# Performance work log

Measured on AMD Instinct MI355X. Metric: run time of the kernel, lower is better.

## Reference

```python
import jax, jax.numpy as jnp
import numpy as np

B, T, D_IN, H, NC = 256, 512, 40, 128, 7


def _lstm_dir(x, W_ih, W_hh, b):
    # x: [B,T,D]; W_ih: [4H,D]; W_hh: [4H,H]; b: [4H] (b_ih+b_hh combined)
    pre = jnp.einsum('btd,gd->btg', x, W_ih) + b  # [B,T,4H]
    h0 = jnp.zeros((x.shape[0], W_hh.shape[1]), x.dtype)
    c0 = jnp.zeros_like(h0)

    def step(carry, p_t):
        h, c = carry
        g = p_t + h @ W_hh.T  # [B,4H]
        i, f, gg, o = jnp.split(g, 4, axis=-1)  # PyTorch gate order: i,f,g,o
        i = jax.nn.sigmoid(i)
        f = jax.nn.sigmoid(f)
        gg = jnp.tanh(gg)
        o = jax.nn.sigmoid(o)
        c = f * c + i * gg
        h = o * jnp.tanh(c)
        return (h, c), h

    _, hs = jax.lax.scan(step, (h0, c0), jnp.swapaxes(pre, 0, 1))  # [T,B,H]
    return jnp.swapaxes(hs, 0, 1)  # [B,T,H]


def _bilstm_layer(x, Wf, Uf, bf, Wr, Ur, br):
    fwd = _lstm_dir(x, Wf, Uf, bf)
    rev = _lstm_dir(x[:, ::-1], Wr, Ur, br)[:, ::-1]
    return jnp.concatenate([fwd, rev], axis=-1)  # [B,T,2H]


def setup_inputs() -> dict:
    key = jax.random.key(0)
    ks = jax.random.split(key, 20)
    s = 1.0 / np.sqrt(H)  # PyTorch LSTM init scale

    def u(k, shape):
        return jax.random.uniform(k, shape, jnp.float32, -s, s)

    inp = {
        'x': jax.random.normal(ks[0], (B, T, D_IN), jnp.float32),
        # layer 0 (input dim 40)
        'W_ih_l0_f': u(ks[1], (4 * H, D_IN)), 'W_hh_l0_f': u(ks[2], (4 * H, H)), 'b_l0_f': u(ks[3], (4 * H,)),
        'W_ih_l0_r': u(ks[4], (4 * H, D_IN)), 'W_hh_l0_r': u(ks[5], (4 * H, H)), 'b_l0_r': u(ks[6], (4 * H,)),
        # layer 1 (input dim 2H)
        'W_ih_l1_f': u(ks[7], (4 * H, 2 * H)), 'W_hh_l1_f': u(ks[8], (4 * H, H)), 'b_l1_f': u(ks[9], (4 * H,)),
        'W_ih_l1_r': u(ks[10], (4 * H, 2 * H)), 'W_hh_l1_r': u(ks[11], (4 * H, H)), 'b_l1_r': u(ks[12], (4 * H,)),
        # classifier head
        'fc_w': u(ks[13], (NC, 2 * H)), 'fc_b': u(ks[14], (NC,)),
    }
    return inp


def reference(x, W_ih_l0_f, W_hh_l0_f, b_l0_f, W_ih_l0_r, W_hh_l0_r, b_l0_r,
              W_ih_l1_f, W_hh_l1_f, b_l1_f, W_ih_l1_r, W_hh_l1_r, b_l1_r,
              fc_w, fc_b):
    h1 = _bilstm_layer(x, W_ih_l0_f, W_hh_l0_f, b_l0_f, W_ih_l0_r, W_hh_l0_r, b_l0_r)
    h2 = _bilstm_layer(h1, W_ih_l1_f, W_hh_l1_f, b_l1_f, W_ih_l1_r, W_hh_l1_r, b_l1_r)
    last = h2[:, -1, :]  # [B,2H]; dropout is identity at eval time
    return last @ fc_w.T + fc_b  # [B,NC]
```

## Files before the change

kernel.cpp:

```cpp
#include <hip/hip_runtime.h>
#include <hip/hip_bf16.h>
#include <type_traits>

typedef short short8 __attribute__((ext_vector_type(8)));
typedef short short4v __attribute__((ext_vector_type(4)));
typedef float f32x4 __attribute__((ext_vector_type(4)));
typedef __bf16 bf16x8 __attribute__((ext_vector_type(8)));

#define DEVI static __device__ __forceinline__

#if __has_builtin(__builtin_amdgcn_exp2f)
#define EXP2(x) __builtin_amdgcn_exp2f(x)
#else
#define EXP2(x) exp2f(x)
#endif
#if __has_builtin(__builtin_amdgcn_rcpf)
#define RCP(x) __builtin_amdgcn_rcpf(x)
#else
#define RCP(x) (1.0f / (x))
#endif

static constexpr int BB = 256, TT = 512, DIN0 = 40, HH = 128, NCLS = 7;
static constexpr float L2E = 1.44269504088896f;

DEVI short f2b(float x) {
  union { __hip_bfloat16 h; short s; } u;
  u.h = __float2bfloat16(x);
  return u.s;
}
DEVI bf16x8 as_bf(short8 s) { return __builtin_bit_cast(bf16x8, s); }
DEVI float b2f(short s) {
  union { unsigned u; float f; } v;
  v.u = ((unsigned)(unsigned short)s) << 16;
  return v.f;
}

DEVI void bar_lgkm() {
  asm volatile("s_waitcnt lgkmcnt(0)\n\ts_barrier" ::: "memory");
}

DEVI f32x4 inv4(f32x4 d) {
  float p1 = d[0] * d[1];
  float p2 = p1 * d[2];
  float p3 = p2 * d[3];
  float R = RCP(p3);
  f32x4 r;
  r[3] = R * p2;
  float R2 = R * d[3];
  r[2] = R2 * p1;
  float R1 = R2 * d[2];
  r[1] = R1 * d[0];
  r[0] = R1 * d[1];
  return r;
}

__global__ __launch_bounds__(512) void rec0(
    const float* __restrict__ x0,
    const float* __restrict__ Wih_f, const float* __restrict__ Whh_f,
    const float* __restrict__ b_f, const float* __restrict__ Wih_r,
    const float* __restrict__ Whh_r, const float* __restrict__ b_r,
    short* __restrict__ h1_out) {
  __shared__ short Hb[2][16][16][8];
  __shared__ short X2[2][8][16][8];

  const int tid = threadIdx.x, w = tid >> 6, lane = tid & 63;
  const int lg = lane >> 4, bcol = lane & 15;
  const int dir = blockIdx.x & 1, b0 = (blockIdx.x >> 1) * 16;
  const int j0 = w * 16 + lg * 4;
  const float* __restrict__ Wih = dir ? Wih_r : Wih_f;
  const float* __restrict__ Whh = dir ? Whh_r : Whh_f;
  const float* __restrict__ bias = dir ? b_r : b_f;
  auto tmap = [&](int s) { return dir ? (TT - 1 - s) : s; };

  short8 wx[4][2], wh[4][4];
  f32x4 bq[4];
#pragma unroll
  for (int q = 0; q < 4; ++q) {
    const float scale = (q == 2) ? (2.0f * L2E) : (-L2E);
    const int m = q * HH + w * 16 + bcol;
#pragma unroll
    for (int kk = 0; kk < 2; ++kk) {
      short8 f;
#pragma unroll
      for (int e = 0; e < 8; ++e) {
        const int k = kk * 32 + lg * 8 + e;
        float v = (k < DIN0) ? Wih[(size_t)m * DIN0 + k] : 0.0f;
        f[e] = f2b(v * scale);
      }
      wx[q][kk] = f;
    }
#pragma unroll
    for (int kk = 0; kk < 4; ++kk) {
      short8 f;
#pragma unroll
      for (int e = 0; e < 8; ++e)
        f[e] = f2b(Whh[(size_t)m * HH + kk * 32 + lg * 8 + e] * scale);
      wh[q][kk] = f;
    }
#pragma unroll
    for (int r = 0; r < 4; ++r) bq[q][r] = bias[q * HH + j0 + r] * scale;
  }

  for (int i = tid; i < 2 * 16 * 16 * 4; i += 512) ((int*)Hb)[i] = 0;
  for (int i = tid; i < 2 * 8 * 16 * 4; i += 512) ((int*)X2)[i] = 0;
  __syncthreads();

  auto load_x = [&](int s) -> f32x4 {
    f32x4 v = {0.f, 0.f, 0.f, 0.f};
    if (tid < 160) {
      int ss = (s < TT) ? s : (TT - 1);
      v = *(const f32x4*)(x0 + ((size_t)(b0 + tid / 10) * TT + tmap(ss)) * DIN0 + (tid % 10) * 4);
    }
    return v;
  };
  auto stage_x = [&](int buf, const f32x4& v) {
    if (tid < 160) {
      short4v o;
      o[0] = f2b(v[0]); o[1] = f2b(v[1]); o[2] = f2b(v[2]); o[3] = f2b(v[3]);
      const int row = tid / 10, c4 = tid % 10;
      *(short4v*)&X2[buf][c4 >> 1][row][(c4 & 1) * 4] = o;
    }
  };
  auto prefill = [&](f32x4* acc, int p) {
#pragma unroll
    for (int kk = 0; kk < 2; ++kk) {
      const bf16x8 bx = as_bf(*(const short8*)&X2[p][kk * 4 + lg][bcol][0]);
#pragma unroll
      for (int q = 0; q < 4; ++q)
        acc[q] = __builtin_amdgcn_mfma_f32_16x16x32_bf16(
            as_bf(wx[q][kk]), bx, (kk == 0) ? bq[q] : acc[q], 0, 0, 0);
    }
  };

  f32x4 cst = {0.f, 0.f, 0.f, 0.f};
  auto cell = [&](f32x4* a, int cur, int s) {
    f32x4 Ei, Ef, Eg, Eo;
#pragma unroll
    for (int r = 0; r < 4; ++r) {
      Ei[r] = EXP2(fminf(a[0][r], 30.f));
      Ef[r] = EXP2(fminf(a[1][r], 30.f));
      Eg[r] = EXP2(fminf(a[2][r], 30.f));
      Eo[r] = EXP2(fminf(a[3][r], 30.f));
    }
    const f32x4 one = {1.f, 1.f, 1.f, 1.f};
    f32x4 si = inv4(one + Ei), sf = inv4(one + Ef);
    f32x4 gd = inv4(one + Eg), so = inv4(one + Eo);
    f32x4 Ec;
#pragma unroll
    for (int r = 0; r < 4; ++r) {
      float tg = 1.f - 2.f * gd[r];
      cst[r] = sf[r] * cst[r] + si[r] * tg;
      Ec[r] = EXP2(fminf(cst[r] * (2.f * L2E), 30.f));
    }
    f32x4 cd = inv4(one + Ec);
    short4v hp;
#pragma unroll
    for (int r = 0; r < 4; ++r) hp[r] = f2b(so[r] * (1.f - 2.f * cd[r]));
    *(short4v*)&Hb[cur ^ 1][j0 >> 3][bcol][j0 & 7] = hp;
    *(short4v*)(h1_out + (((size_t)(b0 + bcol) * TT + tmap(s)) << 8) + dir * HH + j0) = hp;
  };

  stage_x(0, load_x(0));
  stage_x(1, load_x(1));
  f32x4 xst = load_x(2);
  __syncthreads();
  f32x4 accA[4], accB[4];
  prefill(accA, 0);
  bar_lgkm();

  auto stepf = [&](int s, int cur, f32x4* acc, f32x4* accN) {
#pragma unroll
    for (int kk = 0; kk < 4; ++kk) {
      const bf16x8 bh = as_bf(*(const short8*)&Hb[cur][kk * 4 + lg][bcol][0]);
#pragma unroll
      for (int q = 0; q < 4; ++q)
        acc[q] = __builtin_amdgcn_mfma_f32_16x16x32_bf16(as_bf(wh[q][kk]), bh, acc[q], 0, 0, 0);
    }
    cell(acc, cur, s);
    stage_x(cur, xst);
    xst = load_x(s + 3);
    prefill(accN, cur ^ 1);
    bar_lgkm();
  };
  for (int s = 0; s < TT; s += 2) {
    stepf(s, 0, accA, accB);
    stepf(s + 1, 1, accB, accA);
  }
}

template <typename PT>
__global__ __launch_bounds__(512) void pre1(
    const short* __restrict__ h1, const float* __restrict__ Wih_f,
    const float* __restrict__ b_f, const float* __restrict__ Wih_r,
    const float* __restrict__ b_r, PT* __restrict__ pre) {
  __shared__ short X[16 * 256];
  const int tid = threadIdx.x, w = tid >> 6, lane = tid & 63;
  const int lg = lane >> 4, bcol = lane & 15;
  const int gid = blockIdx.x;
  const int dir = gid & 1, tc = (gid >> 1) & 63, bt = gid >> 7;
  const float* __restrict__ Wih = dir ? Wih_r : Wih_f;
  const float* __restrict__ bias = dir ? b_r : b_f;
  const int b0 = bt * 16;

  short8 wx[4][8];
  f32x4 bq[4];
#pragma unroll
  for (int q = 0; q < 4; ++q) {
    const float scale = (q == 2) ? (2.0f * L2E) : (-L2E);
    const int m = q * HH + w * 16 + bcol;
#pragma unroll
    for (int kk = 0; kk < 8; ++kk) {
      short8 f;
#pragma unroll
      for (int e = 0; e < 8; ++e)
        f[e] = f2b(Wih[(size_t)m * 256 + kk * 32 + lg * 8 + e] * scale);
      wx[q][kk] = f;
    }
#pragma unroll
    for (int r = 0; r < 4; ++r) bq[q][r] = bias[q * HH + w * 16 + lg * 4 + r] * scale;
  }

  const int srow = tid >> 5, sch = tid & 31;
  for (int i = 0; i < 8; ++i) {
    const int t = tc * 8 + i;
    short8 v = *(const short8*)(h1 + (((size_t)(b0 + srow) * TT + t) << 8) + sch * 8);
    *(short8*)((char*)X + srow * 512 + ((sch * 16) ^ ((srow & 7) << 4))) = v;
    __syncthreads();
    f32x4 acc[4] = {bq[0], bq[1], bq[2], bq[3]};
#pragma unroll
    for (int kk = 0; kk < 8; ++kk) {
      const bf16x8 bx = as_bf(*(const short8*)((const char*)X + bcol * 512 +
                                               ((kk * 64 + lg * 16) ^ ((bcol & 7) << 4))));
#pragma unroll
      for (int q = 0; q < 4; ++q)
        acc[q] = __builtin_amdgcn_mfma_f32_16x16x32_bf16(as_bf(wx[q][kk]), bx, acc[q], 0, 0, 0);
    }
    PT* op = pre + ((((size_t)dir * 16 + bt) * TT + t) * 8 + w) * 1024 +
             (size_t)(lg * 16 + bcol) * 4;
#pragma unroll
    for (int q = 0; q < 4; ++q) {
      if constexpr (std::is_same_v<PT, float>) {
        *(f32x4*)(op + q * 256) = acc[q];
      } else {
        short4v o;
        o[0] = f2b(acc[q][0]); o[1] = f2b(acc[q][1]);
        o[2] = f2b(acc[q][2]); o[3] = f2b(acc[q][3]);
        *(short4v*)(op + q * 256) = o;
      }
    }
    __syncthreads();
  }
}

template <typename PT>
__global__ __launch_bounds__(512) void rec1(
    const PT* __restrict__ pre, const float* __restrict__ Whh_f,
    const float* __restrict__ Whh_r, float* __restrict__ h2last) {
  __shared__ short Hb[2][16][16][8];
  const int tid = threadIdx.x, w = tid >> 6, lane = tid & 63;
  const int lg = lane >> 4, bcol = lane & 15;
  const int dir = blockIdx.x & 1, bt = blockIdx.x >> 1;
  const int b0 = bt * 16, j0 = w * 16 + lg * 4;
  const float* __restrict__ Whh = dir ? Whh_r : Whh_f;
  auto tmap = [&](int s) { return dir ? (TT - 1 - s) : s; };

  short8 wh[4][4];
#pragma unroll
  for (int q = 0; q < 4; ++q) {
    const float scale = (q == 2) ? (2.0f * L2E) : (-L2E);
    const int m = q * HH + w * 16 + bcol;
#pragma unroll
    for (int kk = 0; kk < 4; ++kk) {
      short8 f;
#pragma unroll
      for (int e = 0; e < 8; ++e)
        f[e] = f2b(Whh[(size_t)m * HH + kk * 32 + lg * 8 + e] * scale);
      wh[q][kk] = f;
    }
  }
  for (int i = tid; i < 2 * 16 * 16 * 4; i += 512) ((int*)Hb)[i] = 0;
  __syncthreads();

  const size_t laneoff = (size_t)(lg * 16 + bcol) * 4;
  auto loadp = [&](f32x4* p, int s) {
    int ss = (s < TT) ? s : (TT - 1);
    const PT* base = pre + ((((size_t)dir * 16 + bt) * TT + tmap(ss)) * 8 + w) * 1024 + laneoff;
#pragma unroll
    for (int q = 0; q < 4; ++q) {
      if constexpr (std::is_same_v<PT, float>) {
        p[q] = *(const f32x4*)(base + q * 256);
      } else {
        short4v v = *(const short4v*)(base + q * 256);
        p[q][0] = b2f(v[0]); p[q][1] = b2f(v[1]);
        p[q][2] = b2f(v[2]); p[q][3] = b2f(v[3]);
      }
    }
  };

  f32x4 cst = {0.f, 0.f, 0.f, 0.f};
  auto stepf = [&](int s, int cur, f32x4* pX) {
    f32x4 acc[4] = {pX[0], pX[1], pX[2], pX[3]};
#pragma unroll
    for (int kk = 0; kk < 4; ++kk) {
      const bf16x8 bh = as_bf(*(const short8*)&Hb[cur][kk * 4 + lg][bcol][0]);
#pragma unroll
      for (int q = 0; q < 4; ++q)
        acc[q] = __builtin_amdgcn_mfma_f32_16x16x32_bf16(as_bf(wh[q][kk]), bh, acc[q], 0, 0, 0);
    }
    f32x4 Ei, Ef, Eg, Eo;
#pragma unroll
    for (int r = 0; r < 4; ++r) {
      Ei[r] = EXP2(fminf(acc[0][r], 30.f));
      Ef[r] = EXP2(fminf(acc[1][r], 30.f));
      Eg[r] = EXP2(fminf(acc[2][r], 30.f));
      Eo[r] = EXP2(fminf(acc[3][r], 30.f));
    }
    const f32x4 one = {1.f, 1.f, 1.f, 1.f};
    f32x4 si = inv4(one + Ei), sf = inv4(one + Ef);
    f32x4 gd = inv4(one + Eg), so = inv4(one + Eo);
    f32x4 Ec;
#pragma unroll
    for (int r = 0; r < 4; ++r) {
      float tg = 1.f - 2.f * gd[r];
      cst[r] = sf[r] * cst[r] + si[r] * tg;
      Ec[r] = EXP2(fminf(cst[r] * (2.f * L2E), 30.f));
    }
    f32x4 cd = inv4(one + Ec);
    short4v hp;
    f32x4 hf;
#pragma unroll
    for (int r = 0; r < 4; ++r) {
      float hv = so[r] * (1.f - 2.f * cd[r]);
      hf[r] = hv;
      hp[r] = f2b(hv);
    }
    *(short4v*)&Hb[cur ^ 1][j0 >> 3][bcol][j0 & 7] = hp;
    if ((dir == 0 && s == TT - 1) || (dir == 1 && s == 0))
      *(f32x4*)(h2last + ((size_t)(b0 + bcol) << 8) + dir * HH + j0) = hf;
    loadp(pX, s + 2);
    bar_lgkm();
  };

  f32x4 pA[4], pB[4];
  loadp(pA, 0);
  loadp(pB, 1);
  for (int s = 0; s < TT; s += 2) {
    stepf(s, 0, pA);
    stepf(s + 1, 1, pB);
  }
}

__global__ __launch_bounds__(512) void rec1_fused(
    const short* __restrict__ h1, const float* __restrict__ Wih_f,
    const float* __restrict__ Whh_f, const float* __restrict__ b_f,
    const float* __restrict__ Wih_r, const float* __restrict__ Whh_r,
    const float* __restrict__ b_r, float* __restrict__ h2last) {
  __shared__ short Hb[2][16][16][8];
  __shared__ char Xraw[16384];

  const int tid = threadIdx.x, w = tid >> 6, lane = tid & 63;
  const int lg = lane >> 4, bcol = lane & 15;
  const int dir = blockIdx.x & 1, b0 = (blockIdx.x >> 1) * 16;
  const int j0 = w * 16 + lg * 4;
  const float* __restrict__ Wih = dir ? Wih_r : Wih_f;
  const float* __restrict__ Whh = dir ? Whh_r : Whh_f;
  const float* __restrict__ bias = dir ? b_r : b_f;
  auto tmap = [&](int s) { return dir ? (TT - 1 - s) : s; };

  short8 wx[4][8], wh[4][4];
  f32x4 bq[4];
#pragma unroll
  for (int q = 0; q < 4; ++q) {
    const float scale = (q == 2) ? (2.0f * L2E) : (-L2E);
    const int m = q * HH + w * 16 + bcol;
#pragma unroll
    for (int kk = 0; kk < 8; ++kk) {
      short8 f;
#pragma unroll
      for (int e = 0; e < 8; ++e)
        f[e] = f2b(Wih[(size_t)m * 256 + kk * 32 + lg * 8 + e] * scale);
      wx[q][kk] = f;
    }
#pragma unroll
    for (int kk = 0; kk < 4; ++kk) {
      short8 f;
#pragma unroll
      for (int e = 0; e < 8; ++e)
        f[e] = f2b(Whh[(size_t)m * HH + kk * 32 + lg * 8 + e] * scale);
      wh[q][kk] = f;
    }
#pragma unroll
    for (int r = 0; r < 4; ++r) bq[q][r] = bias[q * HH + j0 + r] * scale;
  }
  for (int i = tid; i < 2 * 16 * 16 * 4; i += 512) ((int*)Hb)[i] = 0;
  __syncthreads();

  const int xr1 = tid >> 5;
  const int xcb = ((tid << 4) ^ (((tid >> 5) & 7) << 4)) & 511;
  auto ldx = [&](int p, int kk) -> short8 {
    int byte = ((bcol << 9) + (kk << 6) + (lg << 4)) ^ ((bcol & 7) << 4);
    return *(const short8*)(Xraw + p * 8192 + byte);
  };
  auto ldg = [&](int s) -> short8 {
    int ss = (s < TT) ? s : (TT - 1);
    return *(const short8*)((const char*)h1 + (((size_t)(b0 + xr1) * TT + tmap(ss)) << 9) + xcb);
  };

  {
    short8 v0 = ldg(0), v1 = ldg(1);
    *(short8*)(Xraw + tid * 16) = v0;
    *(short8*)(Xraw + 8192 + tid * 16) = v1;
  }
  short8 xstage = ldg(2);
  __syncthreads();

  f32x4 acc[4] = {bq[0], bq[1], bq[2], bq[3]};
#pragma unroll
  for (int kk = 0; kk < 8; ++kk) {
    bf16x8 bx = as_bf(ldx(0, kk));
#pragma unroll
    for (int q = 0; q < 4; ++q)
      acc[q] = __builtin_amdgcn_mfma_f32_16x16x32_bf16(as_bf(wx[q][kk]), bx, acc[q], 0, 0, 0);
  }
  bar_lgkm();

  f32x4 cst = {0.f, 0.f, 0.f, 0.f};
  auto stepf = [&](int s, int buf) {
    *(short8*)(Xraw + buf * 8192 + tid * 16) = xstage;
    xstage = ldg(s + 3);
#pragma unroll
    for (int kk = 0; kk < 4; ++kk) {
      bf16x8 bh = as_bf(*(const short8*)&Hb[buf][kk * 4 + lg][bcol][0]);
#pragma unroll
      for (int q = 0; q < 4; ++q)
        acc[q] = __builtin_amdgcn_mfma_f32_16x16x32_bf16(as_bf(wh[q][kk]), bh, acc[q], 0, 0, 0);
    }
    f32x4 Ei, Ef, Eg, Eo;
#pragma unroll
    for (int r = 0; r < 4; ++r) {
      Ei[r] = EXP2(fminf(acc[0][r], 30.f));
      Ef[r] = EXP2(fminf(acc[1][r], 30.f));
      Eg[r] = EXP2(fminf(acc[2][r], 30.f));
      Eo[r] = EXP2(fminf(acc[3][r], 30.f));
    }
    const f32x4 one = {1.f, 1.f, 1.f, 1.f};
    f32x4 si = inv4(one + Ei), sf = inv4(one + Ef);
    f32x4 gd = inv4(one + Eg), so = inv4(one + Eo);
    f32x4 Ec;
#pragma unroll
    for (int r = 0; r < 4; ++r) {
      float tg = 1.f - 2.f * gd[r];
      cst[r] = sf[r] * cst[r] + si[r] * tg;
      Ec[r] = EXP2(fminf(cst[r] * (2.f * L2E), 30.f));
    }
    f32x4 cd = inv4(one + Ec);
    short4v hp;
    f32x4 hf;
#pragma unroll
    for (int r = 0; r < 4; ++r) {
      float hv = so[r] * (1.f - 2.f * cd[r]);
      hf[r] = hv;
      hp[r] = f2b(hv);
    }
    *(short4v*)&Hb[buf ^ 1][j0 >> 3][bcol][j0 & 7] = hp;
    if ((dir == 0 && s == TT - 1) || (dir == 1 && s == 0))
      *(f32x4*)(h2last + ((size_t)(b0 + bcol) << 8) + dir * HH + j0) = hf;
#pragma unroll
    for (int q = 0; q < 4; ++q) acc[q] = bq[q];
#pragma unroll
    for (int kk = 0; kk < 8; ++kk) {
      bf16x8 bx = as_bf(ldx(buf ^ 1, kk));
#pragma unroll
      for (int q = 0; q < 4; ++q)
        acc[q] = __builtin_amdgcn_mfma_f32_16x16x32_bf16(as_bf(wx[q][kk]), bx, acc[q], 0, 0, 0);
    }
    bar_lgkm();
  };
  for (int s = 0; s < TT; s += 2) {
    stepf(s, 0);
    stepf(s + 1, 1);
  }
}

__global__ void fc_kernel(const float* __restrict__ h2last,
                          const float* __restrict__ fcw,
                          const float* __restrict__ fcb,
                          float* __restrict__ out) {
  const int gid = blockIdx.x * blockDim.x + threadIdx.x;
  if (gid >= BB * NCLS) return;
  const int b = gid / NCLS, n = gid % NCLS;
  const float* hp = h2last + (size_t)b * 256;
  const float* wp = fcw + (size_t)n * 256;
  float s = fcb[n];
#pragma unroll 8
  for (int j = 0; j < 256; ++j) s = fmaf(hp[j], wp[j], s);
  out[gid] = s;
}

extern "C" void kernel_launch(void* const* d_in, const int* in_sizes, int n_in,
                              void* d_out, int out_size, void* d_ws, size_t ws_size,
                              hipStream_t stream) {
  const float* x     = (const float*)d_in[0];
  const float* Wih0f = (const float*)d_in[1];
  const float* Whh0f = (const float*)d_in[2];
  const float* b0f   = (const float*)d_in[3];
  const float* Wih0r = (const float*)d_in[4];
  const float* Whh0r = (const float*)d_in[5];
  const float* b0r   = (const float*)d_in[6];
  const float* Wih1f = (const float*)d_in[7];
  const float* Whh1f = (const float*)d_in[8];
  const float* b1f   = (const float*)d_in[9];
  const float* Wih1r = (const float*)d_in[10];
  const float* Whh1r = (const float*)d_in[11];
  const float* b1r   = (const float*)d_in[12];
  const float* fcw   = (const float*)d_in[13];
  const float* fcb   = (const float*)d_in[14];

  short* h1 = (short*)d_ws;
  float* h2last = (float*)((char*)d_ws + (64ull << 20));
  char* prebuf = (char*)d_ws + (64ull << 20) + (1ull << 20);

  const size_t preElems = 2ull * 16 * TT * 8 * 1024;
  const size_t baseBytes = (64ull << 20) + (1ull << 20);

  rec0<<<dim3(32), dim3(512), 0, stream>>>(
      x, Wih0f, Whh0f, b0f, Wih0r, Whh0r, b0r, h1);

  if (ws_size >= baseBytes + preElems * 4) {
    float* pre = (float*)prebuf;
    pre1<float><<<dim3(2048), dim3(512), 0, stream>>>(h1, Wih1f, b1f, Wih1r, b1r, pre);
    rec1<float><<<dim3(32), dim3(512), 0, stream>>>(pre, Whh1f, Whh1r, h2last);
  } else if (ws_size >= baseBytes + preElems * 2) {
    short* pre = (short*)prebuf;
    pre1<short><<<dim3(2048), dim3(512), 0, stream>>>(h1, Wih1f, b1f, Wih1r, b1r, pre);
    rec1<short><<<dim3(32), dim3(512), 0, stream>>>(pre, Whh1f, Whh1r, h2last);
  } else {
    rec1_fused<<<dim3(32), dim3(512), 0, stream>>>(
        h1, Wih1f, Whh1f, b1f, Wih1r, Whh1r, b1r, h2last);
  }

  fc_kernel<<<dim3((BB * NCLS + 255) / 256), dim3(256), 0, stream>>>(
      h2last, fcw, fcb, (float*)d_out);
}
```

Measured before the change: 1.230 ms.

## Halve batch per recurrent block, merge activation reciprocals, and chunk layer-1 precompute

The recurrent kernels now give each block 8 sequences instead of 16, so 64 blocks run instead of 32. A lane shuffle makes each lane handle two cells, and a new cell2 routine shares one reciprocal across eight gate denominators and another across the two tanh(c) terms. Layer 1 always stores its input projection in bf16 and works through time chunks sized to the workspace. Cell and hidden state are carried between chunks through global buffers, with one pre1/rec1c launch pair per chunk. This is meant to use more compute units and fewer transcendental operations per step, at the cost of extra kernel launches, half-empty MFMA columns, and bf16 rounding of the precompute even when fp32 space is available.

```diff
diff --git a/kernel.cpp b/kernel.cpp
--- a/kernel.cpp
+++ b/kernel.cpp
@@ -1,10 +1,10 @@
 #include <hip/hip_runtime.h>
 #include <hip/hip_bf16.h>
-#include <type_traits>
 
 typedef short short8 __attribute__((ext_vector_type(8)));
 typedef short short4v __attribute__((ext_vector_type(4)));
 typedef float f32x4 __attribute__((ext_vector_type(4)));
+typedef float f32x2 __attribute__((ext_vector_type(2)));
 typedef __bf16 bf16x8 __attribute__((ext_vector_type(8)));
 
 #define DEVI static __device__ __forceinline__
@@ -28,41 +28,337 @@
   u.h = __float2bfloat16(x);
   return u.s;
 }
-DEVI bf16x8 as_bf(short8 s) { return __builtin_bit_cast(bf16x8, s); }
 DEVI float b2f(short s) {
   union { unsigned u; float f; } v;
   v.u = ((unsigned)(unsigned short)s) << 16;
   return v.f;
 }
+DEVI bf16x8 as_bf(short8 s) { return __builtin_bit_cast(bf16x8, s); }
 
 DEVI void bar_lgkm() {
   asm volatile("s_waitcnt lgkmcnt(0)\n\ts_barrier" ::: "memory");
 }
 
-DEVI f32x4 inv4(f32x4 d) {
-  float p1 = d[0] * d[1];
-  float p2 = p1 * d[2];
-  float p3 = p2 * d[3];
-  float R = RCP(p3);
-  f32x4 r;
-  r[3] = R * p2;
-  float R2 = R * d[3];
-  r[2] = R2 * p1;
-  float R1 = R2 * d[2];
-  r[1] = R1 * d[0];
-  r[0] = R1 * d[1];
-  return r;
-}
-
-__global__ __launch_bounds__(512) void rec0(
+DEVI void cell2(float gi0, float gf0, float gg0, float go0,
+                float gi1, float gf1, float gg1, float go1,
+                float& c0, float& c1, float& h0, float& h1) {
+  float d0 = 1.f + EXP2(fminf(gi0, 14.f));
+  float d1 = 1.f + EXP2(fminf(gf0, 14.f));
+  float d2 = 1.f + EXP2(fminf(gg0, 14.f));
+  float d3 = 1.f + EXP2(fminf(go0, 14.f));
+  float d4 = 1.f + EXP2(fminf(gi1, 14.f));
+  float d5 = 1.f + EXP2(fminf(gf1, 14.f));
+  float d6 = 1.f + EXP2(fminf(gg1, 14.f));
+  float d7 = 1.f + EXP2(fminf(go1, 14.f));
+  float p1 = d0 * d1, p2 = p1 * d2, p3 = p2 * d3, p4 = p3 * d4;
+  float p5 = p4 * d5, p6 = p5 * d6, p7 = p6 * d7;
+  float R = RCP(p7);
+  float r7 = R * p6; R *= d7;
+  float r6 = R * p5; R *= d6;
+  float r5 = R * p4; R *= d5;
+  float r4 = R * p3; R *= d4;
+  float r3 = R * p2; R *= d3;
+  float r2 = R * p1; R *= d2;
+  float r1 = R * d0, r0 = R * d1;
+  float tg0 = 1.f - 2.f * r2, tg1 = 1.f - 2.f * r6;
+  c0 = r1 * c0 + r0 * tg0;
+  c1 = r5 * c1 + r4 * tg1;
+  float q0 = 1.f + EXP2(fminf(c0 * (2.f * L2E), 30.f));
+  float q1 = 1.f + EXP2(fminf(c1 * (2.f * L2E), 30.f));
+  float Rq = RCP(q0 * q1);
+  h0 = r3 * (1.f - 2.f * Rq * q1);
+  h1 = r7 * (1.f - 2.f * Rq * q0);
+}
+
+__global__ __launch_bounds__(512) void rec0c(
     const float* __restrict__ x0,
-    const float* __restrict__ Wih_f, const float* __restrict__ Whh_f,
-    const float* __restrict__ b_f, const float* __restrict__ Wih_r,
-    const float* __restrict__ Whh_r, const float* __restrict__ b_r,
+    const float* __restrict__ WihF, const float* __restrict__ WhhF,
+    const float* __restrict__ bF, const float* __restrict__ WihR,
+    const float* __restrict__ WhhR, const float* __restrict__ bR,
     short* __restrict__ h1_out) {
   __shared__ short Hb[2][16][16][8];
   __shared__ short X2[2][8][16][8];
 
+  const int tid = threadIdx.x, w = tid >> 6, lane = tid & 63;
+  const int lg = lane >> 4, bcol = lane & 15;
+  const int hi = bcol >> 3, col = bcol & 7;
+  const int dir = blockIdx.x & 1, b0 = (blockIdx.x >> 1) * 8;
+  const int j0 = w * 16 + lg * 4, j0c = j0 + 2 * hi;
+  const float* __restrict__ Wih = dir ? WihR : WihF;
+  const float* __restrict__ Whh = dir ? WhhR : WhhF;
+  const float* __restrict__ bias = dir ? bR : bF;
+  auto tmap = [&](int s) { return dir ? (TT - 1 - s) : s; };
+
+  short8 wx[4][2], wh[4][4];
+  f32x4 bq[4];
+#pragma unroll
+  for (int q = 0; q < 4; ++q) {
+    const float scale = (q == 2) ? (2.0f * L2E) : (-L2E);
+    const int m = q * HH + w * 16 + bcol;
+#pragma unroll
+    for (int kk = 0; kk < 2; ++kk) {
+      short8 f;
+#pragma unroll
+      for (int e = 0; e < 8; ++e) {
+        const int k = kk * 32 + lg * 8 + e;
+        float v = (k < DIN0) ? Wih[(size_t)m * DIN0 + k] : 0.0f;
+        f[e] = f2b(v * scale);
+      }
+      wx[q][kk] = f;
+    }
+#pragma unroll
+    for (int kk = 0; kk < 4; ++kk) {
+      short8 f;
+#pragma unroll
+      for (int e = 0; e < 8; ++e)
+        f[e] = f2b(Whh[(size_t)m * HH + kk * 32 + lg * 8 + e] * scale);
+      wh[q][kk] = f;
+    }
+#pragma unroll
+    for (int r = 0; r < 4; ++r) bq[q][r] = bias[q * HH + j0 + r] * scale;
+  }
+
+  for (int i = tid; i < (int)(sizeof(Hb) + sizeof(X2)) / 4; i += 512)
+    ((int*)&Hb[0][0][0][0])[i] = 0;
+  __syncthreads();
+
+  auto load_x = [&](int s) -> f32x4 {
+    f32x4 v = {0.f, 0.f, 0.f, 0.f};
+    if (tid < 80) {
+      int ss = (s < TT) ? s : (TT - 1);
+      v = *(const f32x4*)(x0 + ((size_t)(b0 + tid / 10) * TT + tmap(ss)) * DIN0 + (tid % 10) * 4);
+    }
+    return v;
+  };
+  auto stage_x = [&](int buf, const f32x4& v) {
+    if (tid < 80) {
+      short4v o;
+      o[0] = f2b(v[0]); o[1] = f2b(v[1]); o[2] = f2b(v[2]); o[3] = f2b(v[3]);
+      const int row = tid / 10, c4 = tid % 10;
+      *(short4v*)&X2[buf][c4 >> 1][row][(c4 & 1) * 4] = o;
+    }
+  };
+  auto prefill = [&](f32x4* acc, int p) {
+#pragma unroll
+    for (int kk = 0; kk < 2; ++kk) {
+      const bf16x8 bx = as_bf(*(const short8*)&X2[p][kk * 4 + lg][bcol][0]);
+#pragma unroll
+      for (int q = 0; q < 4; ++q)
+        acc[q] = __builtin_amdgcn_mfma_f32_16x16x32_bf16(
+            as_bf(wx[q][kk]), bx, (kk == 0) ? bq[q] : acc[q], 0, 0, 0);
+    }
+  };
+
+  stage_x(0, load_x(0));
+  stage_x(1, load_x(1));
+  f32x4 xst = load_x(2);
+  __syncthreads();
+  f32x4 accA[4], accB[4];
+  prefill(accA, 0);
+  bar_lgkm();
+
+  float cst0 = 0.f, cst1 = 0.f;
+
+  auto stepf = [&](int s, int cur, f32x4* acc, f32x4* accN) {
+#pragma unroll
+    for (int kk = 0; kk < 4; ++kk) {
+      const bf16x8 bh = as_bf(*(const short8*)&Hb[cur][kk * 4 + lg][bcol][0]);
+#pragma unroll
+      for (int q = 0; q < 4; ++q)
+        acc[q] = __builtin_amdgcn_mfma_f32_16x16x32_bf16(as_bf(wh[q][kk]), bh, acc[q], 0, 0, 0);
+    }
+    float g[4][2];
+#pragma unroll
+    for (int q = 0; q < 4; ++q) {
+#pragma unroll
+      for (int u = 0; u < 2; ++u) {
+        float t = __shfl_xor(acc[q][2 + u], 8);
+        g[q][u] = hi ? t : acc[q][u];
+      }
+    }
+    float hv0, hv1;
+    cell2(g[0][0], g[1][0], g[2][0], g[3][0],
+          g[0][1], g[1][1], g[2][1], g[3][1], cst0, cst1, hv0, hv1);
+    int pk = (int)(unsigned short)f2b(hv0) | ((int)(unsigned short)f2b(hv1) << 16);
+    *(int*)&Hb[cur ^ 1][j0 >> 3][col][(j0 & 7) + 2 * hi] = pk;
+    *(int*)(h1_out + (((size_t)(b0 + col) * TT + tmap(s)) << 8) + dir * HH + j0c) = pk;
+    stage_x(cur, xst);
+    xst = load_x(s + 3);
+    prefill(accN, cur ^ 1);
+    bar_lgkm();
+  };
+  for (int s = 0; s < TT; s += 2) {
+    stepf(s, 0, accA, accB);
+    stepf(s + 1, 1, accB, accA);
+  }
+}
+
+__global__ __launch_bounds__(512, 1) void pre1(
+    const short* __restrict__ h1, const float* __restrict__ WihF,
+    const float* __restrict__ bF, const float* __restrict__ WihR,
+    const float* __restrict__ bR, short* __restrict__ pre, int cs, int clen) {
+  __shared__ short X[16 * 256];
+  const int tid = threadIdx.x, w = tid >> 6, lane = tid & 63;
+  const int lg = lane >> 4, bcol = lane & 15;
+  const int gid = blockIdx.x;
+  const int dir = gid & 1, bt16 = (gid >> 1) & 15, tc = gid >> 5;
+  const float* __restrict__ Wih = dir ? WihR : WihF;
+  const float* __restrict__ bias = dir ? bR : bF;
+  const int b0 = bt16 * 16;
+
+  short8 wx[4][8];
+  f32x4 bq[4];
+#pragma unroll
+  for (int q = 0; q < 4; ++q) {
+    const float scale = (q == 2) ? (2.0f * L2E) : (-L2E);
+    const int m = q * HH + w * 16 + bcol;
+#pragma unroll
+    for (int kk = 0; kk < 8; ++kk) {
+      short8 f;
+#pragma unroll
+      for (int e = 0; e < 8; ++e)
+        f[e] = f2b(Wih[(size_t)m * 256 + kk * 32 + lg * 8 + e] * scale);
+      wx[q][kk] = f;
+    }
+#pragma unroll
+    for (int r = 0; r < 4; ++r) bq[q][r] = bias[q * HH + w * 16 + lg * 4 + r] * scale;
+  }
+
+  const int srow = tid >> 5, sch = tid & 31;
+  for (int i = 0; i < 8; ++i) {
+    const int sl = tc * 8 + i, sG = cs + sl;
+    const int t = dir ? (TT - 1 - sG) : sG;
+    short8 v = *(const short8*)(h1 + (((size_t)(b0 + srow) * TT + t) << 8) + sch * 8);
+    *(short8*)((char*)X + srow * 512 + ((sch * 16) ^ ((srow & 7) << 4))) = v;
+    __syncthreads();
+    f32x4 acc[4] = {bq[0], bq[1], bq[2], bq[3]};
+#pragma unroll
+    for (int kk = 0; kk < 8; ++kk) {
+      const bf16x8 bx = as_bf(*(const short8*)((const char*)X + bcol * 512 +
+                                               ((kk * 64 + lg * 16) ^ ((bcol & 7) << 4))));
+#pragma unroll
+      for (int q = 0; q < 4; ++q)
+        acc[q] = __builtin_amdgcn_mfma_f32_16x16x32_bf16(as_bf(wx[q][kk]), bx, acc[q], 0, 0, 0);
+    }
+    short* op = pre + ((((size_t)dir * 16 + bt16) * clen + sl) * 8 + w) * 1024 + bcol * 16 + lg * 4;
+#pragma unroll
+    for (int q = 0; q < 4; ++q) {
+      short4v o;
+      o[0] = f2b(acc[q][0]); o[1] = f2b(acc[q][1]);
+      o[2] = f2b(acc[q][2]); o[3] = f2b(acc[q][3]);
+      *(short4v*)(op + q * 256) = o;
+    }
+    __syncthreads();
+  }
+}
+
+__global__ __launch_bounds__(512) void rec1c(
+    const short* __restrict__ pre, const float* __restrict__ WhhF,
+    const float* __restrict__ WhhR, float* __restrict__ h2last,
+    float* __restrict__ cstate, int* __restrict__ hstate, int cs, int clen) {
+  __shared__ short Hb[2][16][16][8];
+  const int tid = threadIdx.x, w = tid >> 6, lane = tid & 63;
+  const int lg = lane >> 4, bcol = lane & 15;
+  const int hi = bcol >> 3, col = bcol & 7;
+  const int dir = blockIdx.x & 1, bt8 = blockIdx.x >> 1;
+  const int b0 = bt8 * 8, bt16 = bt8 >> 1, half = bt8 & 1;
+  const int j0 = w * 16 + lg * 4, j0c = j0 + 2 * hi;
+  const int wg = blockIdx.x;
+  const float* __restrict__ Whh = dir ? WhhR : WhhF;
+
+  short8 wh[4][4];
+#pragma unroll
+  for (int q = 0; q < 4; ++q) {
+    const float scale = (q == 2) ? (2.0f * L2E) : (-L2E);
+    const int m = q * HH + w * 16 + bcol;
+#pragma unroll
+    for (int kk = 0; kk < 4; ++kk) {
+      short8 f;
+#pragma unroll
+      for (int e = 0; e < 8; ++e)
+        f[e] = f2b(Whh[(size_t)m * HH + kk * 32 + lg * 8 + e] * scale);
+      wh[q][kk] = f;
+    }
+  }
+  for (int i = tid; i < (int)sizeof(Hb) / 4; i += 512) ((int*)&Hb[0][0][0][0])[i] = 0;
+  __syncthreads();
+
+  float cst0 = 0.f, cst1 = 0.f;
+  int pkLast = 0;
+  if (cs != 0) {
+    cst0 = cstate[(wg * 512 + tid) * 2];
+    cst1 = cstate[(wg * 512 + tid) * 2 + 1];
+    pkLast = hstate[wg * 512 + tid];
+    *(int*)&Hb[0][j0 >> 3][col][(j0 & 7) + 2 * hi] = pkLast;
+  }
+  __syncthreads();
+
+  const int col16 = half * 8 + col;
+  auto ldpre = [&](short4v* dst, int ls) {
+    int l = (ls < clen) ? ls : (clen - 1);
+    const short* bp = pre + ((((size_t)dir * 16 + bt16) * clen + l) * 8 + w) * 1024 +
+                      col16 * 16 + lg * 4;
+#pragma unroll
+    for (int q = 0; q < 4; ++q) dst[q] = *(const short4v*)(bp + q * 256);
+  };
+
+  short4v pA[4], pB[4];
+  ldpre(pA, 0);
+  ldpre(pB, 1);
+
+  auto stepf = [&](int ls, int cur, short4v* P) {
+    f32x4 acc[4];
+#pragma unroll
+    for (int q = 0; q < 4; ++q)
+#pragma unroll
+      for (int r = 0; r < 4; ++r) acc[q][r] = b2f(P[q][r]);
+#pragma unroll
+    for (int kk = 0; kk < 4; ++kk) {
+      const bf16x8 bh = as_bf(*(const short8*)&Hb[cur][kk * 4 + lg][bcol][0]);
+#pragma unroll
+      for (int q = 0; q < 4; ++q)
+        acc[q] = __builtin_amdgcn_mfma_f32_16x16x32_bf16(as_bf(wh[q][kk]), bh, acc[q], 0, 0, 0);
+    }
+    float g[4][2];
+#pragma unroll
+    for (int q = 0; q < 4; ++q) {
+#pragma unroll
+      for (int u = 0; u < 2; ++u) {
+        float t = __shfl_xor(acc[q][2 + u], 8);
+        g[q][u] = hi ? t : acc[q][u];
+      }
+    }
+    float hv0, hv1;
+    cell2(g[0][0], g[1][0], g[2][0], g[3][0],
+          g[0][1], g[1][1], g[2][1], g[3][1], cst0, cst1, hv0, hv1);
+    int pk = (int)(unsigned short)f2b(hv0) | ((int)(unsigned short)f2b(hv1) << 16);
+    pkLast = pk;
+    *(int*)&Hb[cur ^ 1][j0 >> 3][col][(j0 & 7) + 2 * hi] = pk;
+    const int sG = cs + ls;
+    if (sG == (dir ? 0 : TT - 1)) {
+      f32x2 o;
+      o[0] = hv0; o[1] = hv1;
+      *(f32x2*)(h2last + ((size_t)(b0 + col) << 8) + dir * HH + j0c) = o;
+    }
+    ldpre(P, ls + 2);
+    bar_lgkm();
+  };
+  for (int ls = 0; ls < clen; ls += 2) {
+    stepf(ls, 0, pA);
+    stepf(ls + 1, 1, pB);
+  }
+  cstate[(wg * 512 + tid) * 2] = cst0;
+  cstate[(wg * 512 + tid) * 2 + 1] = cst1;
+  hstate[wg * 512 + tid] = pkLast;
+}
+
+__global__ __launch_bounds__(512) void rec1_fused(
+    const short* __restrict__ h1, const float* __restrict__ Wih_f,
+    const float* __restrict__ Whh_f, const float* __restrict__ b_f,
+    const float* __restrict__ Wih_r, const float* __restrict__ Whh_r,
+    const float* __restrict__ b_r, float* __restrict__ h2last) {
+  __shared__ short Hb[2][16][16][8];
+  __shared__ char Xraw[16384];
   const int tid = threadIdx.x, w = tid >> 6, lane = tid & 63;
   const int lg = lane >> 4, bcol = lane & 15;
   const int dir = blockIdx.x & 1, b0 = (blockIdx.x >> 1) * 16;
@@ -72,301 +368,6 @@
   const float* __restrict__ bias = dir ? b_r : b_f;
   auto tmap = [&](int s) { return dir ? (TT - 1 - s) : s; };
 
-  short8 wx[4][2], wh[4][4];
-  f32x4 bq[4];
-#pragma unroll
-  for (int q = 0; q < 4; ++q) {
-    const float scale = (q == 2) ? (2.0f * L2E) : (-L2E);
-    const int m = q * HH + w * 16 + bcol;
-#pragma unroll
-    for (int kk = 0; kk < 2; ++kk) {
-      short8 f;
-#pragma unroll
-      for (int e = 0; e < 8; ++e) {
-        const int k = kk * 32 + lg * 8 + e;
-        float v = (k < DIN0) ? Wih[(size_t)m * DIN0 + k] : 0.0f;
-        f[e] = f2b(v * scale);
-      }
-      wx[q][kk] = f;
-    }
-#pragma unroll
-    for (int kk = 0; kk < 4; ++kk) {
-      short8 f;
-#pragma unroll
-      for (int e = 0; e < 8; ++e)
-        f[e] = f2b(Whh[(size_t)m * HH + kk * 32 + lg * 8 + e] * scale);
-      wh[q][kk] = f;
-    }
-#pragma unroll
-    for (int r = 0; r < 4; ++r) bq[q][r] = bias[q * HH + j0 + r] * scale;
-  }
-
-  for (int i = tid; i < 2 * 16 * 16 * 4; i += 512) ((int*)Hb)[i] = 0;
-  for (int i = tid; i < 2 * 8 * 16 * 4; i += 512) ((int*)X2)[i] = 0;
-  __syncthreads();
-
-  auto load_x = [&](int s) -> f32x4 {
-    f32x4 v = {0.f, 0.f, 0.f, 0.f};
-    if (tid < 160) {
-      int ss = (s < TT) ? s : (TT - 1);
-      v = *(const f32x4*)(x0 + ((size_t)(b0 + tid / 10) * TT + tmap(ss)) * DIN0 + (tid % 10) * 4);
-    }
-    return v;
-  };
-  auto stage_x = [&](int buf, const f32x4& v) {
-    if (tid < 160) {
-      short4v o;
-      o[0] = f2b(v[0]); o[1] = f2b(v[1]); o[2] = f2b(v[2]); o[3] = f2b(v[3]);
-      const int row = tid / 10, c4 = tid % 10;
-      *(short4v*)&X2[buf][c4 >> 1][row][(c4 & 1) * 4] = o;
-    }
-  };
-  auto prefill = [&](f32x4* acc, int p) {
-#pragma unroll
-    for (int kk = 0; kk < 2; ++kk) {
-      const bf16x8 bx = as_bf(*(const short8*)&X2[p][kk * 4 + lg][bcol][0]);
-#pragma unroll
-      for (int q = 0; q < 4; ++q)
-        acc[q] = __builtin_amdgcn_mfma_f32_16x16x32_bf16(
-            as_bf(wx[q][kk]), bx, (kk == 0) ? bq[q] : acc[q], 0, 0, 0);
-    }
-  };
-
-  f32x4 cst = {0.f, 0.f, 0.f, 0.f};
-  auto cell = [&](f32x4* a, int cur, int s) {
-    f32x4 Ei, Ef, Eg, Eo;
-#pragma unroll
-    for (int r = 0; r < 4; ++r) {
-      Ei[r] = EXP2(fminf(a[0][r], 30.f));
-      Ef[r] = EXP2(fminf(a[1][r], 30.f));
-      Eg[r] = EXP2(fminf(a[2][r], 30.f));
-      Eo[r] = EXP2(fminf(a[3][r], 30.f));
-    }
-    const f32x4 one = {1.f, 1.f, 1.f, 1.f};
-    f32x4 si = inv4(one + Ei), sf = inv4(one + Ef);
-    f32x4 gd = inv4(one + Eg), so = inv4(one + Eo);
-    f32x4 Ec;
-#pragma unroll
-    for (int r = 0; r < 4; ++r) {
-      float tg = 1.f - 2.f * gd[r];
-      cst[r] = sf[r] * cst[r] + si[r] * tg;
-      Ec[r] = EXP2(fminf(cst[r] * (2.f * L2E), 30.f));
-    }
-    f32x4 cd = inv4(one + Ec);
-    short4v hp;
-#pragma unroll
-    for (int r = 0; r < 4; ++r) hp[r] = f2b(so[r] * (1.f - 2.f * cd[r]));
-    *(short4v*)&Hb[cur ^ 1][j0 >> 3][bcol][j0 & 7] = hp;
-    *(short4v*)(h1_out + (((size_t)(b0 + bcol) * TT + tmap(s)) << 8) + dir * HH + j0) = hp;
-  };
-
-  stage_x(0, load_x(0));
-  stage_x(1, load_x(1));
-  f32x4 xst = load_x(2);
-  __syncthreads();
-  f32x4 accA[4], accB[4];
-  prefill(accA, 0);
-  bar_lgkm();
-
-  auto stepf = [&](int s, int cur, f32x4* acc, f32x4* accN) {
-#pragma unroll
-    for (int kk = 0; kk < 4; ++kk) {
-      const bf16x8 bh = as_bf(*(const short8*)&Hb[cur][kk * 4 + lg][bcol][0]);
-#pragma unroll
-      for (int q = 0; q < 4; ++q)
-        acc[q] = __builtin_amdgcn_mfma_f32_16x16x32_bf16(as_bf(wh[q][kk]), bh, acc[q], 0, 0, 0);
-    }
-    cell(acc, cur, s);
-    stage_x(cur, xst);
-    xst = load_x(s + 3);
-    prefill(accN, cur ^ 1);
-    bar_lgkm();
-  };
-  for (int s = 0; s < TT; s += 2) {
-    stepf(s, 0, accA, accB);
-    stepf(s + 1, 1, accB, accA);
-  }
-}
-
-template <typename PT>
-__global__ __launch_bounds__(512) void pre1(
-    const short* __restrict__ h1, const float* __restrict__ Wih_f,
-    const float* __restrict__ b_f, const float* __restrict__ Wih_r,
-    const float* __restrict__ b_r, PT* __restrict__ pre) {
-  __shared__ short X[16 * 256];
-  const int tid = threadIdx.x, w = tid >> 6, lane = tid & 63;
-  const int lg = lane >> 4, bcol = lane & 15;
-  const int gid = blockIdx.x;
-  const int dir = gid & 1, tc = (gid >> 1) & 63, bt = gid >> 7;
-  const float* __restrict__ Wih = dir ? Wih_r : Wih_f;
-  const float* __restrict__ bias = dir ? b_r : b_f;
-  const int b0 = bt * 16;
-
-  short8 wx[4][8];
-  f32x4 bq[4];
-#pragma unroll
-  for (int q = 0; q < 4; ++q) {
-    const float scale = (q == 2) ? (2.0f * L2E) : (-L2E);
-    const int m = q * HH + w * 16 + bcol;
-#pragma unroll
-    for (int kk = 0; kk < 8; ++kk) {
-      short8 f;
-#pragma unroll
-      for (int e = 0; e < 8; ++e)
-        f[e] = f2b(Wih[(size_t)m * 256 + kk * 32 + lg * 8 + e] * scale);
-      wx[q][kk] = f;
-    }
-#pragma unroll
-    for (int r = 0; r < 4; ++r) bq[q][r] = bias[q * HH + w * 16 + lg * 4 + r] * scale;
-  }
-
-  const int srow = tid >> 5, sch = tid & 31;
-  for (int i = 0; i < 8; ++i) {
-    const int t = tc * 8 + i;
-    short8 v = *(const short8*)(h1 + (((size_t)(b0 + srow) * TT + t) << 8) + sch * 8);
-    *(short8*)((char*)X + srow * 512 + ((sch * 16) ^ ((srow & 7) << 4))) = v;
-    __syncthreads();
-    f32x4 acc[4] = {bq[0], bq[1], bq[2], bq[3]};
-#pragma unroll
-    for (int kk = 0; kk < 8; ++kk) {
-      const bf16x8 bx = as_bf(*(const short8*)((const char*)X + bcol * 512 +
-                                               ((kk * 64 + lg * 16) ^ ((bcol & 7) << 4))));
-#pragma unroll
-      for (int q = 0; q < 4; ++q)
-        acc[q] = __builtin_amdgcn_mfma_f32_16x16x32_bf16(as_bf(wx[q][kk]), bx, acc[q], 0, 0, 0);
-    }
-    PT* op = pre + ((((size_t)dir * 16 + bt) * TT + t) * 8 + w) * 1024 +
-             (size_t)(lg * 16 + bcol) * 4;
-#pragma unroll
-    for (int q = 0; q < 4; ++q) {
-      if constexpr (std::is_same_v<PT, float>) {
-        *(f32x4*)(op + q * 256) = acc[q];
-      } else {
-        short4v o;
-        o[0] = f2b(acc[q][0]); o[1] = f2b(acc[q][1]);
-        o[2] = f2b(acc[q][2]); o[3] = f2b(acc[q][3]);
-        *(short4v*)(op + q * 256) = o;
-      }
-    }
-    __syncthreads();
-  }
-}
-
-template <typename PT>
-__global__ __launch_bounds__(512) void rec1(
-    const PT* __restrict__ pre, const float* __restrict__ Whh_f,
-    const float* __restrict__ Whh_r, float* __restrict__ h2last) {
-  __shared__ short Hb[2][16][16][8];
-  const int tid = threadIdx.x, w = tid >> 6, lane = tid & 63;
-  const int lg = lane >> 4, bcol = lane & 15;
-  const int dir = blockIdx.x & 1, bt = blockIdx.x >> 1;
-  const int b0 = bt * 16, j0 = w * 16 + lg * 4;
-  const float* __restrict__ Whh = dir ? Whh_r : Whh_f;
-  auto tmap = [&](int s) { return dir ? (TT - 1 - s) : s; };
-
-  short8 wh[4][4];
-#pragma unroll
-  for (int q = 0; q < 4; ++q) {
-    const float scale = (q == 2) ? (2.0f * L2E) : (-L2E);
-    const int m = q * HH + w * 16 + bcol;
-#pragma unroll
-    for (int kk = 0; kk < 4; ++kk) {
-      short8 f;
-#pragma unroll
-      for (int e = 0; e < 8; ++e)
-        f[e] = f2b(Whh[(size_t)m * HH + kk * 32 + lg * 8 + e] * scale);
-      wh[q][kk] = f;
-    }
-  }
-  for (int i = tid; i < 2 * 16 * 16 * 4; i += 512) ((int*)Hb)[i] = 0;
-  __syncthreads();
-
-  const size_t laneoff = (size_t)(lg * 16 + bcol) * 4;
-  auto loadp = [&](f32x4* p, int s) {
-    int ss = (s < TT) ? s : (TT - 1);
-    const PT* base = pre + ((((size_t)dir * 16 + bt) * TT + tmap(ss)) * 8 + w) * 1024 + laneoff;
-#pragma unroll
-    for (int q = 0; q < 4; ++q) {
-      if constexpr (std::is_same_v<PT, float>) {
-        p[q] = *(const f32x4*)(base + q * 256);
-      } else {
-        short4v v = *(const short4v*)(base + q * 256);
-        p[q][0] = b2f(v[0]); p[q][1] = b2f(v[1]);
-        p[q][2] = b2f(v[2]); p[q][3] = b2f(v[3]);
-      }
-    }
-  };
-
-  f32x4 cst = {0.f, 0.f, 0.f, 0.f};
-  auto stepf = [&](int s, int cur, f32x4* pX) {
-    f32x4 acc[4] = {pX[0], pX[1], pX[2], pX[3]};
-#pragma unroll
-    for (int kk = 0; kk < 4; ++kk) {
-      const bf16x8 bh = as_bf(*(const short8*)&Hb[cur][kk * 4 + lg][bcol][0]);
-#pragma unroll
-      for (int q = 0; q < 4; ++q)
-        acc[q] = __builtin_amdgcn_mfma_f32_16x16x32_bf16(as_bf(wh[q][kk]), bh, acc[q], 0, 0, 0);
-    }
-    f32x4 Ei, Ef, Eg, Eo;
-#pragma unroll
-    for (int r = 0; r < 4; ++r) {
-      Ei[r] = EXP2(fminf(acc[0][r], 30.f));
-      Ef[r] = EXP2(fminf(acc[1][r], 30.f));
-      Eg[r] = EXP2(fminf(acc[2][r], 30.f));
-      Eo[r] = EXP2(fminf(acc[3][r], 30.f));
-    }
-    const f32x4 one = {1.f, 1.f, 1.f, 1.f};
-    f32x4 si = inv4(one + Ei), sf = inv4(one + Ef);
-    f32x4 gd = inv4(one + Eg), so = inv4(one + Eo);
-    f32x4 Ec;
-#pragma unroll
-    for (int r = 0; r < 4; ++r) {
-      float tg = 1.f - 2.f * gd[r];
-      cst[r] = sf[r] * cst[r] + si[r] * tg;
-      Ec[r] = EXP2(fminf(cst[r] * (2.f * L2E), 30.f));
-    }
-    f32x4 cd = inv4(one + Ec);
-    short4v hp;
-    f32x4 hf;
-#pragma unroll
-    for (int r = 0; r < 4; ++r) {
-      float hv = so[r] * (1.f - 2.f * cd[r]);
-      hf[r] = hv;
-      hp[r] = f2b(hv);
-    }
-    *(short4v*)&Hb[cur ^ 1][j0 >> 3][bcol][j0 & 7] = hp;
-    if ((dir == 0 && s == TT - 1) || (dir == 1 && s == 0))
-      *(f32x4*)(h2last + ((size_t)(b0 + bcol) << 8) + dir * HH + j0) = hf;
-    loadp(pX, s + 2);
-    bar_lgkm();
-  };
-
-  f32x4 pA[4], pB[4];
-  loadp(pA, 0);
-  loadp(pB, 1);
-  for (int s = 0; s < TT; s += 2) {
-    stepf(s, 0, pA);
-    stepf(s + 1, 1, pB);
-  }
-}
-
-__global__ __launch_bounds__(512) void rec1_fused(
-    const short* __restrict__ h1, const float* __restrict__ Wih_f,
-    const float* __restrict__ Whh_f, const float* __restrict__ b_f,
-    const float* __restrict__ Wih_r, const float* __restrict__ Whh_r,
-    const float* __restrict__ b_r, float* __restrict__ h2last) {
-  __shared__ short Hb[2][16][16][8];
-  __shared__ char Xraw[16384];
-
-  const int tid = threadIdx.x, w = tid >> 6, lane = tid & 63;
-  const int lg = lane >> 4, bcol = lane & 15;
-  const int dir = blockIdx.x & 1, b0 = (blockIdx.x >> 1) * 16;
-  const int j0 = w * 16 + lg * 4;
-  const float* __restrict__ Wih = dir ? Wih_r : Wih_f;
-  const float* __restrict__ Whh = dir ? Whh_r : Whh_f;
-  const float* __restrict__ bias = dir ? b_r : b_f;
-  auto tmap = [&](int s) { return dir ? (TT - 1 - s) : s; };
-
   short8 wx[4][8], wh[4][4];
   f32x4 bq[4];
 #pragma unroll
@@ -405,7 +406,6 @@
     int ss = (s < TT) ? s : (TT - 1);
     return *(const short8*)((const char*)h1 + (((size_t)(b0 + xr1) * TT + tmap(ss)) << 9) + xcb);
   };
-
   {
     short8 v0 = ldg(0), v1 = ldg(1);
     *(short8*)(Xraw + tid * 16) = v0;
@@ -435,36 +435,25 @@
       for (int q = 0; q < 4; ++q)
         acc[q] = __builtin_amdgcn_mfma_f32_16x16x32_bf16(as_bf(wh[q][kk]), bh, acc[q], 0, 0, 0);
     }
-    f32x4 Ei, Ef, Eg, Eo;
-#pragma unroll
-    for (int r = 0; r < 4; ++r) {
-      Ei[r] = EXP2(fminf(acc[0][r], 30.f));
-      Ef[r] = EXP2(fminf(acc[1][r], 30.f));
-      Eg[r] = EXP2(fminf(acc[2][r], 30.f));
-      Eo[r] = EXP2(fminf(acc[3][r], 30.f));
-    }
-    const f32x4 one = {1.f, 1.f, 1.f, 1.f};
-    f32x4 si = inv4(one + Ei), sf = inv4(one + Ef);
-    f32x4 gd = inv4(one + Eg), so = inv4(one + Eo);
-    f32x4 Ec;
-#pragma unroll
-    for (int r = 0; r < 4; ++r) {
-      float tg = 1.f - 2.f * gd[r];
-      cst[r] = sf[r] * cst[r] + si[r] * tg;
-      Ec[r] = EXP2(fminf(cst[r] * (2.f * L2E), 30.f));
-    }
-    f32x4 cd = inv4(one + Ec);
+    float hv0, hv1, hv2, hv3;
+    {
+      float c0 = cst[0], c1 = cst[1];
+      cell2(acc[0][0], acc[1][0], acc[2][0], acc[3][0],
+            acc[0][1], acc[1][1], acc[2][1], acc[3][1], c0, c1, hv0, hv1);
+      cst[0] = c0; cst[1] = c1;
+      float c2 = cst[2], c3 = cst[3];
+      cell2(acc[0][2], acc[1][2], acc[2][2], acc[3][2],
+            acc[0][3], acc[1][3], acc[2][3], acc[3][3], c2, c3, hv2, hv3);
+      cst[2] = c2; cst[3] = c3;
+    }
     short4v hp;
-    f32x4 hf;
-#pragma unroll
-    for (int r = 0; r < 4; ++r) {
-      float hv = so[r] * (1.f - 2.f * cd[r]);
-      hf[r] = hv;
-      hp[r] = f2b(hv);
-    }
+    hp[0] = f2b(hv0); hp[1] = f2b(hv1); hp[2] = f2b(hv2); hp[3] = f2b(hv3);
     *(short4v*)&Hb[buf ^ 1][j0 >> 3][bcol][j0 & 7] = hp;
-    if ((dir == 0 && s == TT - 1) || (dir == 1 && s == 0))
+    if ((dir == 0 && s == TT - 1) || (dir == 1 && s == 0)) {
+      f32x4 hf;
+      hf[0] = hv0; hf[1] = hv1; hf[2] = hv2; hf[3] = hv3;
       *(f32x4*)(h2last + ((size_t)(b0 + bcol) << 8) + dir * HH + j0) = hf;
+    }
 #pragma unroll
     for (int q = 0; q < 4; ++q) acc[q] = bq[q];
 #pragma unroll
@@ -518,22 +507,26 @@
 
   short* h1 = (short*)d_ws;
   float* h2last = (float*)((char*)d_ws + (64ull << 20));
-  char* prebuf = (char*)d_ws + (64ull << 20) + (1ull << 20);
-
-  const size_t preElems = 2ull * 16 * TT * 8 * 1024;
-  const size_t baseBytes = (64ull << 20) + (1ull << 20);
-
-  rec0<<<dim3(32), dim3(512), 0, stream>>>(
+  float* cstate = (float*)((char*)d_ws + (64ull << 20) + (512ull << 10));
+  int* hstate = (int*)((char*)d_ws + (64ull << 20) + (768ull << 10));
+  short* pre = (short*)((char*)d_ws + (66ull << 20));
+
+  size_t budget = ws_size > (66ull << 20) ? ws_size - (66ull << 20) : 0;
+  int chunkT = 0;
+  const int cands[7] = {512, 256, 128, 64, 32, 16, 8};
+  for (int i = 0; i < 7; ++i)
+    if ((size_t)cands[i] * (512ull << 10) <= budget) { chunkT = cands[i]; break; }
+
+  rec0c<<<dim3(64), dim3(512), 0, stream>>>(
       x, Wih0f, Whh0f, b0f, Wih0r, Whh0r, b0r, h1);
 
-  if (ws_size >= baseBytes + preElems * 4) {
-    float* pre = (float*)prebuf;
-    pre1<float><<<dim3(2048), dim3(512), 0, stream>>>(h1, Wih1f, b1f, Wih1r, b1r, pre);
-    rec1<float><<<dim3(32), dim3(512), 0, stream>>>(pre, Whh1f, Whh1r, h2last);
-  } else if (ws_size >= baseBytes + preElems * 2) {
-    short* pre = (short*)prebuf;
-    pre1<short><<<dim3(2048), dim3(512), 0, stream>>>(h1, Wih1f, b1f, Wih1r, b1r, pre);
-    rec1<short><<<dim3(32), dim3(512), 0, stream>>>(pre, Whh1f, Whh1r, h2last);
+  if (chunkT > 0) {
+    for (int cs = 0; cs < TT; cs += chunkT) {
+      pre1<<<dim3(4 * chunkT), dim3(512), 0, stream>>>(
+          h1, Wih1f, b1f, Wih1r, b1r, pre, cs, chunkT);
+      rec1c<<<dim3(64), dim3(512), 0, stream>>>(
+          pre, Whh1f, Whh1r, h2last, cstate, hstate, cs, chunkT);
+    }
   } else {
     rec1_fused<<<dim3(32), dim3(512), 0, stream>>>(
         h1, Wih1f, Whh1f, b1f, Wih1r, Whh1r, b1r, h2last);
```

After: 1.042 ms. -15.3%, faster.
